# Kernel tuning notes

Measured on AMD Instinct MI355X. Metric: run time of the kernel, lower is better.

## Reference

```python
import jax, jax.numpy as jnp
import numpy as np

N, E, F_IN, H, C, L = 50000, 800000, 128, 128, 47, 3
BN_EPS = 1e-5


def setup_inputs() -> dict:
    key = jax.random.key(0)
    ks = jax.random.split(key, 12)
    s = 0.1
    return {
        "x": jax.random.normal(ks[0], (N, F_IN), jnp.float32),
        "edge_index": jax.random.randint(ks[1], (2, E), 0, N, jnp.int32),
        # stacked GINConv MLP params (in_channels == hidden so all layers stack)
        "W1": jax.random.normal(ks[2], (L, F_IN, H), jnp.float32) * s,
        "b1": jnp.full((L, H), 0.01, jnp.float32),
        "gamma": jnp.ones((L, H), jnp.float32),
        "beta": jnp.zeros((L, H), jnp.float32),
        "bn_mean": jnp.zeros((L, H), jnp.float32),
        "bn_var": jnp.ones((L, H), jnp.float32),
        "W2": jax.random.normal(ks[3], (L, H, H), jnp.float32) * s,
        "b2": jnp.full((L, H), 0.01, jnp.float32),
        # head
        "lw1": jax.random.normal(ks[4], (H, H), jnp.float32) * s,
        "lb1": jnp.zeros((H,), jnp.float32),
        "lw2": jax.random.normal(ks[5], (H, C), jnp.float32) * s,
        "lb2": jnp.zeros((C,), jnp.float32),
    }


def reference(x, edge_index, W1, b1, gamma, beta, bn_mean, bn_var, W2, b2, lw1, lb1, lw2, lb2):
    src, dst = edge_index[0], edge_index[1]
    h = x
    for i in range(L):
        # GINConv: nn((1 + eps) * x + sum_{j in N(i)} x_j), eps = 0
        agg = jax.ops.segment_sum(h[src], dst, num_segments=N)  # [N, H] scatter-sum
        z = agg + h
        z = z @ W1[i] + b1[i]
        # BatchNorm1d in eval mode (running stats)
        z = (z - bn_mean[i]) * jax.lax.rsqrt(bn_var[i] + BN_EPS) * gamma[i] + beta[i]
        z = jax.nn.relu(z)
        h = jax.nn.relu(z @ W2[i] + b2[i])
    h = jax.nn.relu(h @ lw1 + lb1)
    # dropout disabled (eval mode)
    logits = h @ lw2 + lb2
    return jax.nn.log_softmax(logits, axis=-1)
```

## Files before the change

### kernel.cpp

```cpp
#include <hip/hip_runtime.h>
#include <math.h>

#define NN 50000
#define EE 800000
#define HH 128
#define LL 3
#define CC 47
#define CAP 64
#define FILL_B 2048
#define NT_TILES 782

typedef _Float16 half8 __attribute__((ext_vector_type(8)));
typedef float    f32x4 __attribute__((ext_vector_type(4)));

__device__ __forceinline__ f32x4 mfma16(half8 a, half8 b, f32x4 c) {
    return __builtin_amdgcn_mfma_f32_16x16x32_f16(a, b, c, 0, 0, 0);
}

__global__ void k_fill_prep(const int* __restrict__ ei, int* __restrict__ cursor,
                            unsigned short* __restrict__ csr,
                            const float* __restrict__ x, const float* __restrict__ W1,
                            const float* __restrict__ W2, const float* __restrict__ lw1,
                            const float* __restrict__ lw2, const float* __restrict__ b1,
                            const float* __restrict__ gamma, const float* __restrict__ beta,
                            const float* __restrict__ bnm, const float* __restrict__ bnv,
                            _Float16* __restrict__ xh, _Float16* __restrict__ Wt1h,
                            _Float16* __restrict__ Wt2h, _Float16* __restrict__ lw1t,
                            _Float16* __restrict__ lw2t, float* __restrict__ A1f,
                            float* __restrict__ B1f) {
    if (blockIdx.x < FILL_B) {
        const int part = blockIdx.x & 7;
        const int chunk = blockIdx.x >> 3;
        const int nchunks = FILL_B >> 3;
        const int lo = part * (NN / 8);
        const int hi = (part == 7) ? NN : lo + (NN / 8);
        for (int e = chunk * 256 + threadIdx.x; e < EE; e += nchunks * 256) {
            const int d = ei[EE + e];
            if (d >= lo && d < hi) {
                const int pos = atomicAdd(&cursor[d], 1);
                if (pos < CAP) csr[(d << 6) + pos] = (unsigned short)ei[e];
            }
        }
        return;
    }
    long i = (long)(blockIdx.x - FILL_B) * 256 + threadIdx.x;
    const long P0 = (long)NN * HH;
    const long P1 = P0 + (long)LL * HH * HH;
    const long P2 = P1 + (long)LL * HH * HH;
    const long P3 = P2 + HH * HH;
    const long P4 = P3 + 48 * HH;
    const long P5 = P4 + LL * HH;
    if (i < P0) {
        xh[i] = (_Float16)x[i];
    } else if (i < P1) {
        long j = i - P0;
        int l = (int)(j / (HH * HH));
        int n = (int)((j / HH) % HH);
        int k = (int)(j % HH);
        Wt1h[l * HH * HH + n * HH + k] = (_Float16)W1[l * HH * HH + k * HH + n];
    } else if (i < P2) {
        long j = i - P1;
        int l = (int)(j / (HH * HH));
        int n = (int)((j / HH) % HH);
        int k = (int)(j % HH);
        Wt2h[l * HH * HH + n * HH + k] = (_Float16)W2[l * HH * HH + k * HH + n];
    } else if (i < P3) {
        long j = i - P2;
        int n = (int)(j / HH), k = (int)(j % HH);
        lw1t[n * HH + k] = (_Float16)lw1[k * HH + n];
    } else if (i < P4) {
        long j = i - P3;
        int n = (int)(j / HH), k = (int)(j % HH);
        lw2t[n * HH + k] = (_Float16)((n < CC) ? lw2[k * CC + n] : 0.f);
    } else if (i < P5) {
        long j = i - P4;
        float s = gamma[j] * rsqrtf(bnv[j] + 1e-5f);
        A1f[j] = s;
        B1f[j] = (b1[j] - bnm[j]) * s + beta[j];
    }
}

__global__ __launch_bounds__(256, 4) void k_layer(
    const _Float16* __restrict__ hin, _Float16* __restrict__ hout,
    const _Float16* __restrict__ Wt1, const _Float16* __restrict__ Wt2,
    const float* __restrict__ A1, const float* __restrict__ B1,
    const float* __restrict__ b2, const int* __restrict__ degs,
    const unsigned short* __restrict__ csr) {
    __shared__ _Float16 Ab[64 * 136];
    const int tid = threadIdx.x;
    const int wave = tid >> 6, lane = tid & 63;
    const int q = lane >> 4, l15 = lane & 15;
    const int tile0 = blockIdx.x * 64;
    const int fo = (tid & 15) * 8;

    half8 Bf[2][4];
#pragma unroll
    for (int t = 0; t < 2; ++t)
#pragma unroll
        for (int kt = 0; kt < 4; ++kt)
            Bf[t][kt] = *(const half8*)(Wt1 + (wave * 32 + t * 16 + l15) * 128 + kt * 32 + q * 8);

#pragma unroll
    for (int pass = 0; pass < 4; ++pass) {
        const int r = pass * 16 + (tid >> 4);
        const int g = tile0 + r;
        float a[8];
        if (g < NN) {
            half8 hv = *(const half8*)(hin + (size_t)g * HH + fo);
#pragma unroll
            for (int j = 0; j < 8; ++j) a[j] = (float)hv[j];
            int d = degs[g];
            d = (d < CAP) ? d : CAP;
            const int e0 = g << 6;
#pragma unroll 4
            for (int e = e0; e < e0 + d; ++e) {
                const int s = (int)csr[e];
                half8 v = *(const half8*)(hin + (size_t)s * HH + fo);
#pragma unroll
                for (int j = 0; j < 8; ++j) a[j] += (float)v[j];
            }
        } else {
#pragma unroll
            for (int j = 0; j < 8; ++j) a[j] = 0.f;
        }
        half8 o;
#pragma unroll
        for (int j = 0; j < 8; ++j) o[j] = (_Float16)a[j];
        *(half8*)(Ab + r * 136 + fo) = o;
    }
    __syncthreads();

    f32x4 acc[4][2];
#pragma unroll
    for (int s = 0; s < 4; ++s)
#pragma unroll
        for (int t = 0; t < 2; ++t) acc[s][t] = (f32x4){0.f, 0.f, 0.f, 0.f};
#pragma unroll
    for (int kt = 0; kt < 4; ++kt) {
        const int ko = kt * 32 + q * 8;
        half8 a0 = *(const half8*)(Ab + (0 * 16 + l15) * 136 + ko);
        half8 a1 = *(const half8*)(Ab + (1 * 16 + l15) * 136 + ko);
        half8 a2 = *(const half8*)(Ab + (2 * 16 + l15) * 136 + ko);
        half8 a3 = *(const half8*)(Ab + (3 * 16 + l15) * 136 + ko);
        acc[0][0] = mfma16(a0, Bf[0][kt], acc[0][0]);
        acc[1][0] = mfma16(a1, Bf[0][kt], acc[1][0]);
        acc[2][0] = mfma16(a2, Bf[0][kt], acc[2][0]);
        acc[3][0] = mfma16(a3, Bf[0][kt], acc[3][0]);
        acc[0][1] = mfma16(a0, Bf[1][kt], acc[0][1]);
        acc[1][1] = mfma16(a1, Bf[1][kt], acc[1][1]);
        acc[2][1] = mfma16(a2, Bf[1][kt], acc[2][1]);
        acc[3][1] = mfma16(a3, Bf[1][kt], acc[3][1]);
    }
#pragma unroll
    for (int t = 0; t < 2; ++t)
#pragma unroll
        for (int kt = 0; kt < 4; ++kt)
            Bf[t][kt] = *(const half8*)(Wt2 + (wave * 32 + t * 16 + l15) * 128 + kt * 32 + q * 8);
    __syncthreads();

#pragma unroll
    for (int t = 0; t < 2; ++t) {
        const int col = wave * 32 + t * 16 + l15;
        const float sc = A1[col], sh = B1[col];
#pragma unroll
        for (int s = 0; s < 4; ++s)
#pragma unroll
            for (int r = 0; r < 4; ++r) {
                const int row = s * 16 + q * 4 + r;
                float v = acc[s][t][r] * sc + sh;
                Ab[row * 136 + col] = (_Float16)fmaxf(v, 0.f);
            }
    }
    __syncthreads();

#pragma unroll
    for (int s = 0; s < 4; ++s)
#pragma unroll
        for (int t = 0; t < 2; ++t) acc[s][t] = (f32x4){0.f, 0.f, 0.f, 0.f};
#pragma unroll
    for (int kt = 0; kt < 4; ++kt) {
        const int ko = kt * 32 + q * 8;
        half8 a0 = *(const half8*)(Ab + (0 * 16 + l15) * 136 + ko);
        half8 a1 = *(const half8*)(Ab + (1 * 16 + l15) * 136 + ko);
        half8 a2 = *(const half8*)(Ab + (2 * 16 + l15) * 136 + ko);
        half8 a3 = *(const half8*)(Ab + (3 * 16 + l15) * 136 + ko);
        acc[0][0] = mfma16(a0, Bf[0][kt], acc[0][0]);
        acc[1][0] = mfma16(a1, Bf[0][kt], acc[1][0]);
        acc[2][0] = mfma16(a2, Bf[0][kt], acc[2][0]);
        acc[3][0] = mfma16(a3, Bf[0][kt], acc[3][0]);
        acc[0][1] = mfma16(a0, Bf[1][kt], acc[0][1]);
        acc[1][1] = mfma16(a1, Bf[1][kt], acc[1][1]);
        acc[2][1] = mfma16(a2, Bf[1][kt], acc[2][1]);
        acc[3][1] = mfma16(a3, Bf[1][kt], acc[3][1]);
    }
#pragma unroll
    for (int t = 0; t < 2; ++t) {
        const int col = wave * 32 + t * 16 + l15;
        const float bb = b2[col];
#pragma unroll
        for (int s = 0; s < 4; ++s)
#pragma unroll
            for (int r = 0; r < 4; ++r) {
                const int row = s * 16 + q * 4 + r;
                const int g = tile0 + row;
                if (g < NN) {
                    float v = fmaxf(acc[s][t][r] + bb, 0.f);
                    hout[(size_t)g * HH + col] = (_Float16)v;
                }
            }
    }
}

__global__ __launch_bounds__(256, 4) void k_layer_head(
    const _Float16* __restrict__ hin,
    const _Float16* __restrict__ Wt1, const _Float16* __restrict__ Wt2,
    const float* __restrict__ A1, const float* __restrict__ B1,
    const float* __restrict__ b2,
    const _Float16* __restrict__ lw1t, const _Float16* __restrict__ lw2t,
    const float* __restrict__ lb1, const float* __restrict__ lb2,
    float* __restrict__ out, const int* __restrict__ degs,
    const unsigned short* __restrict__ csr) {
    __shared__ _Float16 Ab[64 * 136];
    const int tid = threadIdx.x;
    const int wave = tid >> 6, lane = tid & 63;
    const int q = lane >> 4, l15 = lane & 15;
    const int tile0 = blockIdx.x * 64;
    const int fo = (tid & 15) * 8;

    half8 Bf[2][4];
#pragma unroll
    for (int t = 0; t < 2; ++t)
#pragma unroll
        for (int kt = 0; kt < 4; ++kt)
            Bf[t][kt] = *(const half8*)(Wt1 + (wave * 32 + t * 16 + l15) * 128 + kt * 32 + q * 8);

#pragma unroll
    for (int pass = 0; pass < 4; ++pass) {
        const int r = pass * 16 + (tid >> 4);
        const int g = tile0 + r;
        float a[8];
        if (g < NN) {
            half8 hv = *(const half8*)(hin + (size_t)g * HH + fo);
#pragma unroll
            for (int j = 0; j < 8; ++j) a[j] = (float)hv[j];
            int d = degs[g];
            d = (d < CAP) ? d : CAP;
            const int e0 = g << 6;
#pragma unroll 4
            for (int e = e0; e < e0 + d; ++e) {
                const int s = (int)csr[e];
                half8 v = *(const half8*)(hin + (size_t)s * HH + fo);
#pragma unroll
                for (int j = 0; j < 8; ++j) a[j] += (float)v[j];
            }
        } else {
#pragma unroll
            for (int j = 0; j < 8; ++j) a[j] = 0.f;
        }
        half8 o;
#pragma unroll
        for (int j = 0; j < 8; ++j) o[j] = (_Float16)a[j];
        *(half8*)(Ab + r * 136 + fo) = o;
    }
    __syncthreads();

    f32x4 acc[4][2];
#pragma unroll
    for (int s = 0; s < 4; ++s)
#pragma unroll
        for (int t = 0; t < 2; ++t) acc[s][t] = (f32x4){0.f, 0.f, 0.f, 0.f};
#pragma unroll
    for (int kt = 0; kt < 4; ++kt) {
        const int ko = kt * 32 + q * 8;
        half8 a0 = *(const half8*)(Ab + (0 * 16 + l15) * 136 + ko);
        half8 a1 = *(const half8*)(Ab + (1 * 16 + l15) * 136 + ko);
        half8 a2 = *(const half8*)(Ab + (2 * 16 + l15) * 136 + ko);
        half8 a3 = *(const half8*)(Ab + (3 * 16 + l15) * 136 + ko);
        acc[0][0] = mfma16(a0, Bf[0][kt], acc[0][0]);
        acc[1][0] = mfma16(a1, Bf[0][kt], acc[1][0]);
        acc[2][0] = mfma16(a2, Bf[0][kt], acc[2][0]);
        acc[3][0] = mfma16(a3, Bf[0][kt], acc[3][0]);
        acc[0][1] = mfma16(a0, Bf[1][kt], acc[0][1]);
        acc[1][1] = mfma16(a1, Bf[1][kt], acc[1][1]);
        acc[2][1] = mfma16(a2, Bf[1][kt], acc[2][1]);
        acc[3][1] = mfma16(a3, Bf[1][kt], acc[3][1]);
    }
#pragma unroll
    for (int t = 0; t < 2; ++t)
#pragma unroll
        for (int kt = 0; kt < 4; ++kt)
            Bf[t][kt] = *(const half8*)(Wt2 + (wave * 32 + t * 16 + l15) * 128 + kt * 32 + q * 8);
    __syncthreads();
#pragma unroll
    for (int t = 0; t < 2; ++t) {
        const int col = wave * 32 + t * 16 + l15;
        const float sc = A1[col], sh = B1[col];
#pragma unroll
        for (int s = 0; s < 4; ++s)
#pragma unroll
            for (int r = 0; r < 4; ++r) {
                const int row = s * 16 + q * 4 + r;
                float v = acc[s][t][r] * sc + sh;
                Ab[row * 136 + col] = (_Float16)fmaxf(v, 0.f);
            }
    }
    __syncthreads();

#pragma unroll
    for (int s = 0; s < 4; ++s)
#pragma unroll
        for (int t = 0; t < 2; ++t) acc[s][t] = (f32x4){0.f, 0.f, 0.f, 0.f};
#pragma unroll
    for (int kt = 0; kt < 4; ++kt) {
        const int ko = kt * 32 + q * 8;
        half8 a0 = *(const half8*)(Ab + (0 * 16 + l15) * 136 + ko);
        half8 a1 = *(const half8*)(Ab + (1 * 16 + l15) * 136 + ko);
        half8 a2 = *(const half8*)(Ab + (2 * 16 + l15) * 136 + ko);
        half8 a3 = *(const half8*)(Ab + (3 * 16 + l15) * 136 + ko);
        acc[0][0] = mfma16(a0, Bf[0][kt], acc[0][0]);
        acc[1][0] = mfma16(a1, Bf[0][kt], acc[1][0]);
        acc[2][0] = mfma16(a2, Bf[0][kt], acc[2][0]);
        acc[3][0] = mfma16(a3, Bf[0][kt], acc[3][0]);
        acc[0][1] = mfma16(a0, Bf[1][kt], acc[0][1]);
        acc[1][1] = mfma16(a1, Bf[1][kt], acc[1][1]);
        acc[2][1] = mfma16(a2, Bf[1][kt], acc[2][1]);
        acc[3][1] = mfma16(a3, Bf[1][kt], acc[3][1]);
    }
#pragma unroll
    for (int t = 0; t < 2; ++t)
#pragma unroll
        for (int kt = 0; kt < 4; ++kt)
            Bf[t][kt] = *(const half8*)(lw1t + (wave * 32 + t * 16 + l15) * 128 + kt * 32 + q * 8);
    __syncthreads();
#pragma unroll
    for (int t = 0; t < 2; ++t) {
        const int col = wave * 32 + t * 16 + l15;
        const float bb = b2[col];
#pragma unroll
        for (int s = 0; s < 4; ++s)
#pragma unroll
            for (int r = 0; r < 4; ++r) {
                const int row = s * 16 + q * 4 + r;
                Ab[row * 136 + col] = (_Float16)fmaxf(acc[s][t][r] + bb, 0.f);
            }
    }
    __syncthreads();

#pragma unroll
    for (int s = 0; s < 4; ++s)
#pragma unroll
        for (int t = 0; t < 2; ++t) acc[s][t] = (f32x4){0.f, 0.f, 0.f, 0.f};
#pragma unroll
    for (int kt = 0; kt < 4; ++kt) {
        const int ko = kt * 32 + q * 8;
        half8 a0 = *(const half8*)(Ab + (0 * 16 + l15) * 136 + ko);
        half8 a1 = *(const half8*)(Ab + (1 * 16 + l15) * 136 + ko);
        half8 a2 = *(const half8*)(Ab + (2 * 16 + l15) * 136 + ko);
        half8 a3 = *(const half8*)(Ab + (3 * 16 + l15) * 136 + ko);
        acc[0][0] = mfma16(a0, Bf[0][kt], acc[0][0]);
        acc[1][0] = mfma16(a1, Bf[0][kt], acc[1][0]);
        acc[2][0] = mfma16(a2, Bf[0][kt], acc[2][0]);
        acc[3][0] = mfma16(a3, Bf[0][kt], acc[3][0]);
        acc[0][1] = mfma16(a0, Bf[1][kt], acc[0][1]);
        acc[1][1] = mfma16(a1, Bf[1][kt], acc[1][1]);
        acc[2][1] = mfma16(a2, Bf[1][kt], acc[2][1]);
        acc[3][1] = mfma16(a3, Bf[1][kt], acc[3][1]);
    }
    half8 Bh[4];
    if (wave < 3) {
#pragma unroll
        for (int kt = 0; kt < 4; ++kt)
            Bh[kt] = *(const half8*)(lw2t + (wave * 16 + l15) * 128 + kt * 32 + q * 8);
    }
    __syncthreads();
#pragma unroll
    for (int t = 0; t < 2; ++t) {
        const int col = wave * 32 + t * 16 + l15;
        const float bb = lb1[col];
#pragma unroll
        for (int s = 0; s < 4; ++s)
#pragma unroll
            for (int r = 0; r < 4; ++r) {
                const int row = s * 16 + q * 4 + r;
                Ab[row * 136 + col] = (_Float16)fmaxf(acc[s][t][r] + bb, 0.f);
            }
    }
    __syncthreads();

    f32x4 acc2[4];
#pragma unroll
    for (int s = 0; s < 4; ++s) acc2[s] = (f32x4){0.f, 0.f, 0.f, 0.f};
    if (wave < 3) {
#pragma unroll
        for (int kt = 0; kt < 4; ++kt) {
            const int ko = kt * 32 + q * 8;
            half8 a0 = *(const half8*)(Ab + (0 * 16 + l15) * 136 + ko);
            half8 a1 = *(const half8*)(Ab + (1 * 16 + l15) * 136 + ko);
            half8 a2 = *(const half8*)(Ab + (2 * 16 + l15) * 136 + ko);
            half8 a3 = *(const half8*)(Ab + (3 * 16 + l15) * 136 + ko);
            acc2[0] = mfma16(a0, Bh[kt], acc2[0]);
            acc2[1] = mfma16(a1, Bh[kt], acc2[1]);
            acc2[2] = mfma16(a2, Bh[kt], acc2[2]);
            acc2[3] = mfma16(a3, Bh[kt], acc2[3]);
        }
    }
    __syncthreads();

    float* Lb = (float*)Ab;
    if (wave < 3) {
        const int col = wave * 16 + l15;
        const float bb = (col < CC) ? lb2[col] : 0.f;
#pragma unroll
        for (int s = 0; s < 4; ++s)
#pragma unroll
            for (int r = 0; r < 4; ++r) {
                const int row = s * 16 + q * 4 + r;
                Lb[row * 49 + col] = acc2[s][r] + bb;
            }
    }
    __syncthreads();

    if (tid < 64) {
        const int g = tile0 + tid;
        if (g < NN) {
            float mx = -1e30f;
            for (int c = 0; c < CC; ++c) mx = fmaxf(mx, Lb[tid * 49 + c]);
            float ssum = 0.f;
            for (int c = 0; c < CC; ++c) ssum += expf(Lb[tid * 49 + c] - mx);
            const float ls = logf(ssum) + mx;
            for (int c = 0; c < CC; ++c) out[(size_t)g * CC + c] = Lb[tid * 49 + c] - ls;
        }
    }
}

extern "C" void kernel_launch(void* const* d_in, const int* in_sizes, int n_in,
                              void* d_out, int out_size, void* d_ws, size_t ws_size,
                              hipStream_t stream) {
    const float* x     = (const float*)d_in[0];
    const int*   ei    = (const int*)d_in[1];
    const float* W1    = (const float*)d_in[2];
    const float* b1    = (const float*)d_in[3];
    const float* gamma = (const float*)d_in[4];
    const float* beta  = (const float*)d_in[5];
    const float* bnm   = (const float*)d_in[6];
    const float* bnv   = (const float*)d_in[7];
    const float* W2    = (const float*)d_in[8];
    const float* b2    = (const float*)d_in[9];
    const float* lw1   = (const float*)d_in[10];
    const float* lb1   = (const float*)d_in[11];
    const float* lw2   = (const float*)d_in[12];
    const float* lb2   = (const float*)d_in[13];
    float* out = (float*)d_out;

    char* p = (char*)d_ws;
    auto carve = [&](size_t bytes) -> char* {
        char* r = p;
        p += (bytes + 255) & ~(size_t)255;
        return r;
    };
    int* cursor = (int*)carve((size_t)NN * 4);
    unsigned short* csr = (unsigned short*)carve((size_t)NN * CAP * 2);
    _Float16* Wt1h = (_Float16*)carve((size_t)LL * HH * HH * 2);
    _Float16* Wt2h = (_Float16*)carve((size_t)LL * HH * HH * 2);
    _Float16* lw1t = (_Float16*)carve((size_t)HH * HH * 2);
    _Float16* lw2t = (_Float16*)carve((size_t)48 * HH * 2);
    float* A1f = (float*)carve((size_t)LL * HH * 4);
    float* B1f = (float*)carve((size_t)LL * HH * 4);
    _Float16* xh  = (_Float16*)carve((size_t)NN * HH * 2);
    _Float16* hb0 = (_Float16*)carve((size_t)NN * HH * 2);
    _Float16* hb1 = (_Float16*)carve((size_t)NN * HH * 2);

    hipMemsetAsync(cursor, 0, (size_t)NN * 4, stream);
    const long prep_total = (long)NN * HH + 2L * LL * HH * HH + (long)HH * HH + 48L * HH + (long)LL * HH;
    const int prep_blocks = (int)((prep_total + 255) / 256);
    k_fill_prep<<<FILL_B + prep_blocks, 256, 0, stream>>>(
        ei, cursor, csr, x, W1, W2, lw1, lw2, b1, gamma, beta, bnm, bnv,
        xh, Wt1h, Wt2h, lw1t, lw2t, A1f, B1f);

    k_layer<<<NT_TILES, 256, 0, stream>>>(xh, hb0, Wt1h, Wt2h, A1f, B1f, b2,
                                          cursor, csr);
    k_layer<<<NT_TILES, 256, 0, stream>>>(hb0, hb1, Wt1h + HH * HH, Wt2h + HH * HH,
                                          A1f + HH, B1f + HH, b2 + HH,
                                          cursor, csr);
    k_layer_head<<<NT_TILES, 256, 0, stream>>>(hb1, Wt1h + 2 * HH * HH, Wt2h + 2 * HH * HH,
                                               A1f + 2 * HH, B1f + 2 * HH, b2 + 2 * HH,
                                               lw1t, lw2t, lb1, lb2, out,
                                               cursor, csr);
}
```

Before: 275.3 us.

## Halve node tile, batch neighbor gathers by four with zero sentinel row

Shrinks each block's node tile from 64 to 32 rows, doubling the number of blocks and raising the launch-bounds occupancy hint, so more blocks run concurrently to hide gather latency. The neighbor aggregation now reads four CSR indices at once and issues four independent row loads per step. Out-of-range slots point at an extra zero row appended to each feature buffer, which the prep kernel clears. The x-to-half conversion is also vectorized to eight elements per thread. The trade-off is that each block reloads the weight fragments for half as many rows, and padded slots cost wasted loads.

```diff
diff --git a/kernel.cpp b/kernel.cpp
--- a/kernel.cpp
+++ b/kernel.cpp
@@ -8,10 +8,12 @@
 #define CC 47
 #define CAP 64
 #define FILL_B 2048
-#define NT_TILES 782
+#define TILE 32
+#define NT_TILES 1563
 
 typedef _Float16 half8 __attribute__((ext_vector_type(8)));
 typedef float    f32x4 __attribute__((ext_vector_type(4)));
+typedef unsigned short us4 __attribute__((ext_vector_type(4)));
 
 __device__ __forceinline__ f32x4 mfma16(half8 a, half8 b, f32x4 c) {
     return __builtin_amdgcn_mfma_f32_16x16x32_f16(a, b, c, 0, 0, 0);
@@ -24,7 +26,8 @@
                             const float* __restrict__ lw2, const float* __restrict__ b1,
                             const float* __restrict__ gamma, const float* __restrict__ beta,
                             const float* __restrict__ bnm, const float* __restrict__ bnv,
-                            _Float16* __restrict__ xh, _Float16* __restrict__ Wt1h,
+                            _Float16* __restrict__ xh, _Float16* __restrict__ hb0,
+                            _Float16* __restrict__ hb1, _Float16* __restrict__ Wt1h,
                             _Float16* __restrict__ Wt2h, _Float16* __restrict__ lw1t,
                             _Float16* __restrict__ lw2t, float* __restrict__ A1f,
                             float* __restrict__ B1f) {
@@ -43,54 +46,65 @@
         }
         return;
     }
-    long i = (long)(blockIdx.x - FILL_B) * 256 + threadIdx.x;
-    const long P0 = (long)NN * HH;
-    const long P1 = P0 + (long)LL * HH * HH;
-    const long P2 = P1 + (long)LL * HH * HH;
-    const long P3 = P2 + HH * HH;
-    const long P4 = P3 + 48 * HH;
-    const long P5 = P4 + LL * HH;
-    if (i < P0) {
-        xh[i] = (_Float16)x[i];
-    } else if (i < P1) {
-        long j = i - P0;
-        int l = (int)(j / (HH * HH));
-        int n = (int)((j / HH) % HH);
-        int k = (int)(j % HH);
+    const int i = (blockIdx.x - FILL_B) * 256 + threadIdx.x;
+    const int Q0 = (NN * HH) / 8;
+    const int Q1 = Q0 + LL * HH * HH;
+    const int Q2 = Q1 + LL * HH * HH;
+    const int Q3 = Q2 + HH * HH;
+    const int Q4 = Q3 + 48 * HH;
+    const int Q5 = Q4 + LL * HH;
+    const int Q6 = Q5 + 3 * HH;
+    if (i < Q0) {
+        const f32x4* xp = (const f32x4*)x + (size_t)i * 2;
+        f32x4 u = xp[0], v = xp[1];
+        half8 o;
+        o[0] = (_Float16)u[0]; o[1] = (_Float16)u[1]; o[2] = (_Float16)u[2]; o[3] = (_Float16)u[3];
+        o[4] = (_Float16)v[0]; o[5] = (_Float16)v[1]; o[6] = (_Float16)v[2]; o[7] = (_Float16)v[3];
+        *((half8*)xh + i) = o;
+    } else if (i < Q1) {
+        int j = i - Q0;
+        int l = j / (HH * HH);
+        int n = (j / HH) % HH;
+        int k = j % HH;
         Wt1h[l * HH * HH + n * HH + k] = (_Float16)W1[l * HH * HH + k * HH + n];
-    } else if (i < P2) {
-        long j = i - P1;
-        int l = (int)(j / (HH * HH));
-        int n = (int)((j / HH) % HH);
-        int k = (int)(j % HH);
+    } else if (i < Q2) {
+        int j = i - Q1;
+        int l = j / (HH * HH);
+        int n = (j / HH) % HH;
+        int k = j % HH;
         Wt2h[l * HH * HH + n * HH + k] = (_Float16)W2[l * HH * HH + k * HH + n];
-    } else if (i < P3) {
-        long j = i - P2;
-        int n = (int)(j / HH), k = (int)(j % HH);
+    } else if (i < Q3) {
+        int j = i - Q2;
+        int n = j / HH, k = j % HH;
         lw1t[n * HH + k] = (_Float16)lw1[k * HH + n];
-    } else if (i < P4) {
-        long j = i - P3;
-        int n = (int)(j / HH), k = (int)(j % HH);
+    } else if (i < Q4) {
+        int j = i - Q3;
+        int n = j / HH, k = j % HH;
         lw2t[n * HH + k] = (_Float16)((n < CC) ? lw2[k * CC + n] : 0.f);
-    } else if (i < P5) {
-        long j = i - P4;
+    } else if (i < Q5) {
+        int j = i - Q4;
         float s = gamma[j] * rsqrtf(bnv[j] + 1e-5f);
         A1f[j] = s;
         B1f[j] = (b1[j] - bnm[j]) * s + beta[j];
+    } else if (i < Q6) {
+        int j = i - Q5;
+        int b = j >> 7, k = j & 127;
+        _Float16* t = (b == 0) ? xh : ((b == 1) ? hb0 : hb1);
+        t[(size_t)NN * HH + k] = (_Float16)0.f;
     }
 }
 
-__global__ __launch_bounds__(256, 4) void k_layer(
+__global__ __launch_bounds__(256, 6) void k_layer(
     const _Float16* __restrict__ hin, _Float16* __restrict__ hout,
     const _Float16* __restrict__ Wt1, const _Float16* __restrict__ Wt2,
     const float* __restrict__ A1, const float* __restrict__ B1,
     const float* __restrict__ b2, const int* __restrict__ degs,
     const unsigned short* __restrict__ csr) {
-    __shared__ _Float16 Ab[64 * 136];
+    __shared__ _Float16 Ab[TILE * 136];
     const int tid = threadIdx.x;
     const int wave = tid >> 6, lane = tid & 63;
     const int q = lane >> 4, l15 = lane & 15;
-    const int tile0 = blockIdx.x * 64;
+    const int tile0 = blockIdx.x * TILE;
     const int fo = (tid & 15) * 8;
 
     half8 Bf[2][4];
@@ -101,27 +115,30 @@
             Bf[t][kt] = *(const half8*)(Wt1 + (wave * 32 + t * 16 + l15) * 128 + kt * 32 + q * 8);
 
 #pragma unroll
-    for (int pass = 0; pass < 4; ++pass) {
+    for (int pass = 0; pass < 2; ++pass) {
         const int r = pass * 16 + (tid >> 4);
         const int g = tile0 + r;
+        const int gg = (g < NN) ? g : NN;
         float a[8];
-        if (g < NN) {
-            half8 hv = *(const half8*)(hin + (size_t)g * HH + fo);
-#pragma unroll
-            for (int j = 0; j < 8; ++j) a[j] = (float)hv[j];
-            int d = degs[g];
-            d = (d < CAP) ? d : CAP;
-            const int e0 = g << 6;
-#pragma unroll 4
-            for (int e = e0; e < e0 + d; ++e) {
-                const int s = (int)csr[e];
-                half8 v = *(const half8*)(hin + (size_t)s * HH + fo);
-#pragma unroll
-                for (int j = 0; j < 8; ++j) a[j] += (float)v[j];
-            }
-        } else {
-#pragma unroll
-            for (int j = 0; j < 8; ++j) a[j] = 0.f;
+        half8 hv = *(const half8*)(hin + (size_t)gg * HH + fo);
+#pragma unroll
+        for (int j = 0; j < 8; ++j) a[j] = (float)hv[j];
+        int d = (g < NN) ? degs[g] : 0;
+        d = (d < CAP) ? d : CAP;
+        const int e0 = gg << 6;
+        for (int c = 0; c < d; c += 4) {
+            us4 sv = *(const us4*)(csr + e0 + c);
+            const int s0 = (int)sv[0];
+            const int s1 = (c + 1 < d) ? (int)sv[1] : NN;
+            const int s2 = (c + 2 < d) ? (int)sv[2] : NN;
+            const int s3 = (c + 3 < d) ? (int)sv[3] : NN;
+            half8 v0 = *(const half8*)(hin + (size_t)s0 * HH + fo);
+            half8 v1 = *(const half8*)(hin + (size_t)s1 * HH + fo);
+            half8 v2 = *(const half8*)(hin + (size_t)s2 * HH + fo);
+            half8 v3 = *(const half8*)(hin + (size_t)s3 * HH + fo);
+#pragma unroll
+            for (int j = 0; j < 8; ++j)
+                a[j] += ((float)v0[j] + (float)v1[j]) + ((float)v2[j] + (float)v3[j]);
         }
         half8 o;
 #pragma unroll
@@ -130,9 +147,9 @@
     }
     __syncthreads();
 
-    f32x4 acc[4][2];
-#pragma unroll
-    for (int s = 0; s < 4; ++s)
+    f32x4 acc[2][2];
+#pragma unroll
+    for (int s = 0; s < 2; ++s)
 #pragma unroll
         for (int t = 0; t < 2; ++t) acc[s][t] = (f32x4){0.f, 0.f, 0.f, 0.f};
 #pragma unroll
@@ -140,16 +157,10 @@
         const int ko = kt * 32 + q * 8;
         half8 a0 = *(const half8*)(Ab + (0 * 16 + l15) * 136 + ko);
         half8 a1 = *(const half8*)(Ab + (1 * 16 + l15) * 136 + ko);
-        half8 a2 = *(const half8*)(Ab + (2 * 16 + l15) * 136 + ko);
-        half8 a3 = *(const half8*)(Ab + (3 * 16 + l15) * 136 + ko);
         acc[0][0] = mfma16(a0, Bf[0][kt], acc[0][0]);
         acc[1][0] = mfma16(a1, Bf[0][kt], acc[1][0]);
-        acc[2][0] = mfma16(a2, Bf[0][kt], acc[2][0]);
-        acc[3][0] = mfma16(a3, Bf[0][kt], acc[3][0]);
         acc[0][1] = mfma16(a0, Bf[1][kt], acc[0][1]);
         acc[1][1] = mfma16(a1, Bf[1][kt], acc[1][1]);
-        acc[2][1] = mfma16(a2, Bf[1][kt], acc[2][1]);
-        acc[3][1] = mfma16(a3, Bf[1][kt], acc[3][1]);
     }
 #pragma unroll
     for (int t = 0; t < 2; ++t)
@@ -163,7 +174,7 @@
         const int col = wave * 32 + t * 16 + l15;
         const float sc = A1[col], sh = B1[col];
 #pragma unroll
-        for (int s = 0; s < 4; ++s)
+        for (int s = 0; s < 2; ++s)
 #pragma unroll
             for (int r = 0; r < 4; ++r) {
                 const int row = s * 16 + q * 4 + r;
@@ -174,7 +185,7 @@
     __syncthreads();
 
 #pragma unroll
-    for (int s = 0; s < 4; ++s)
+    for (int s = 0; s < 2; ++s)
 #pragma unroll
         for (int t = 0; t < 2; ++t) acc[s][t] = (f32x4){0.f, 0.f, 0.f, 0.f};
 #pragma unroll
@@ -182,23 +193,17 @@
         const int ko = kt * 32 + q * 8;
         half8 a0 = *(const half8*)(Ab + (0 * 16 + l15) * 136 + ko);
         half8 a1 = *(const half8*)(Ab + (1 * 16 + l15) * 136 + ko);
-        half8 a2 = *(const half8*)(Ab + (2 * 16 + l15) * 136 + ko);
-        half8 a3 = *(const half8*)(Ab + (3 * 16 + l15) * 136 + ko);
         acc[0][0] = mfma16(a0, Bf[0][kt], acc[0][0]);
         acc[1][0] = mfma16(a1, Bf[0][kt], acc[1][0]);
-        acc[2][0] = mfma16(a2, Bf[0][kt], acc[2][0]);
-        acc[3][0] = mfma16(a3, Bf[0][kt], acc[3][0]);
         acc[0][1] = mfma16(a0, Bf[1][kt], acc[0][1]);
         acc[1][1] = mfma16(a1, Bf[1][kt], acc[1][1]);
-        acc[2][1] = mfma16(a2, Bf[1][kt], acc[2][1]);
-        acc[3][1] = mfma16(a3, Bf[1][kt], acc[3][1]);
     }
 #pragma unroll
     for (int t = 0; t < 2; ++t) {
         const int col = wave * 32 + t * 16 + l15;
         const float bb = b2[col];
 #pragma unroll
-        for (int s = 0; s < 4; ++s)
+        for (int s = 0; s < 2; ++s)
 #pragma unroll
             for (int r = 0; r < 4; ++r) {
                 const int row = s * 16 + q * 4 + r;
@@ -211,7 +216,7 @@
     }
 }
 
-__global__ __launch_bounds__(256, 4) void k_layer_head(
+__global__ __launch_bounds__(256, 6) void k_layer_head(
     const _Float16* __restrict__ hin,
     const _Float16* __restrict__ Wt1, const _Float16* __restrict__ Wt2,
     const float* __restrict__ A1, const float* __restrict__ B1,
@@ -220,11 +225,11 @@
     const float* __restrict__ lb1, const float* __restrict__ lb2,
     float* __restrict__ out, const int* __restrict__ degs,
     const unsigned short* __restrict__ csr) {
-    __shared__ _Float16 Ab[64 * 136];
+    __shared__ _Float16 Ab[TILE * 136];
     const int tid = threadIdx.x;
     const int wave = tid >> 6, lane = tid & 63;
     const int q = lane >> 4, l15 = lane & 15;
-    const int tile0 = blockIdx.x * 64;
+    const int tile0 = blockIdx.x * TILE;
     const int fo = (tid & 15) * 8;
 
     half8 Bf[2][4];
@@ -235,27 +240,30 @@
             Bf[t][kt] = *(const half8*)(Wt1 + (wave * 32 + t * 16 + l15) * 128 + kt * 32 + q * 8);
 
 #pragma unroll
-    for (int pass = 0; pass < 4; ++pass) {
+    for (int pass = 0; pass < 2; ++pass) {
         const int r = pass * 16 + (tid >> 4);
         const int g = tile0 + r;
+        const int gg = (g < NN) ? g : NN;
         float a[8];
-        if (g < NN) {
-            half8 hv = *(const half8*)(hin + (size_t)g * HH + fo);
-#pragma unroll
-            for (int j = 0; j < 8; ++j) a[j] = (float)hv[j];
-            int d = degs[g];
-            d = (d < CAP) ? d : CAP;
-            const int e0 = g << 6;
-#pragma unroll 4
-            for (int e = e0; e < e0 + d; ++e) {
-                const int s = (int)csr[e];
-                half8 v = *(const half8*)(hin + (size_t)s * HH + fo);
-#pragma unroll
-                for (int j = 0; j < 8; ++j) a[j] += (float)v[j];
-            }
-        } else {
-#pragma unroll
-            for (int j = 0; j < 8; ++j) a[j] = 0.f;
+        half8 hv = *(const half8*)(hin + (size_t)gg * HH + fo);
+#pragma unroll
+        for (int j = 0; j < 8; ++j) a[j] = (float)hv[j];
+        int d = (g < NN) ? degs[g] : 0;
+        d = (d < CAP) ? d : CAP;
+        const int e0 = gg << 6;
+        for (int c = 0; c < d; c += 4) {
+            us4 sv = *(const us4*)(csr + e0 + c);
+            const int s0 = (int)sv[0];
+            const int s1 = (c + 1 < d) ? (int)sv[1] : NN;
+            const int s2 = (c + 2 < d) ? (int)sv[2] : NN;
+            const int s3 = (c + 3 < d) ? (int)sv[3] : NN;
+            half8 v0 = *(const half8*)(hin + (size_t)s0 * HH + fo);
+            half8 v1 = *(const half8*)(hin + (size_t)s1 * HH + fo);
+            half8 v2 = *(const half8*)(hin + (size_t)s2 * HH + fo);
+            half8 v3 = *(const half8*)(hin + (size_t)s3 * HH + fo);
+#pragma unroll
+            for (int j = 0; j < 8; ++j)
+                a[j] += ((float)v0[j] + (float)v1[j]) + ((float)v2[j] + (float)v3[j]);
         }
         half8 o;
 #pragma unroll
@@ -264,9 +272,9 @@
     }
     __syncthreads();
 
-    f32x4 acc[4][2];
-#pragma unroll
-    for (int s = 0; s < 4; ++s)
+    f32x4 acc[2][2];
+#pragma unroll
+    for (int s = 0; s < 2; ++s)
 #pragma unroll
         for (int t = 0; t < 2; ++t) acc[s][t] = (f32x4){0.f, 0.f, 0.f, 0.f};
 #pragma unroll
@@ -274,16 +282,10 @@
         const int ko = kt * 32 + q * 8;
         half8 a0 = *(const half8*)(Ab + (0 * 16 + l15) * 136 + ko);
         half8 a1 = *(const half8*)(Ab + (1 * 16 + l15) * 136 + ko);
-        half8 a2 = *(const half8*)(Ab + (2 * 16 + l15) * 136 + ko);
-        half8 a3 = *(const half8*)(Ab + (3 * 16 + l15) * 136 + ko);
         acc[0][0] = mfma16(a0, Bf[0][kt], acc[0][0]);
         acc[1][0] = mfma16(a1, Bf[0][kt], acc[1][0]);
-        acc[2][0] = mfma16(a2, Bf[0][kt], acc[2][0]);
-        acc[3][0] = mfma16(a3, Bf[0][kt], acc[3][0]);
         acc[0][1] = mfma16(a0, Bf[1][kt], acc[0][1]);
         acc[1][1] = mfma16(a1, Bf[1][kt], acc[1][1]);
-        acc[2][1] = mfma16(a2, Bf[1][kt], acc[2][1]);
-        acc[3][1] = mfma16(a3, Bf[1][kt], acc[3][1]);
     }
 #pragma unroll
     for (int t = 0; t < 2; ++t)
@@ -296,7 +298,7 @@
         const int col = wave * 32 + t * 16 + l15;
         const float sc = A1[col], sh = B1[col];
 #pragma unroll
-        for (int s = 0; s < 4; ++s)
+        for (int s = 0; s < 2; ++s)
 #pragma unroll
             for (int r = 0; r < 4; ++r) {
                 const int row = s * 16 + q * 4 + r;
@@ -307,7 +309,7 @@
     __syncthreads();
 
 #pragma unroll
-    for (int s = 0; s < 4; ++s)
+    for (int s = 0; s < 2; ++s)
 #pragma unroll
         for (int t = 0; t < 2; ++t) acc[s][t] = (f32x4){0.f, 0.f, 0.f, 0.f};
 #pragma unroll
@@ -315,16 +317,10 @@
         const int ko = kt * 32 + q * 8;
         half8 a0 = *(const half8*)(Ab + (0 * 16 + l15) * 136 + ko);
         half8 a1 = *(const half8*)(Ab + (1 * 16 + l15) * 136 + ko);
-        half8 a2 = *(const half8*)(Ab + (2 * 16 + l15) * 136 + ko);
-        half8 a3 = *(const half8*)(Ab + (3 * 16 + l15) * 136 + ko);
         acc[0][0] = mfma16(a0, Bf[0][kt], acc[0][0]);
         acc[1][0] = mfma16(a1, Bf[0][kt], acc[1][0]);
-        acc[2][0] = mfma16(a2, Bf[0][kt], acc[2][0]);
-        acc[3][0] = mfma16(a3, Bf[0][kt], acc[3][0]);
         acc[0][1] = mfma16(a0, Bf[1][kt], acc[0][1]);
         acc[1][1] = mfma16(a1, Bf[1][kt], acc[1][1]);
-        acc[2][1] = mfma16(a2, Bf[1][kt], acc[2][1]);
-        acc[3][1] = mfma16(a3, Bf[1][kt], acc[3][1]);
     }
 #pragma unroll
     for (int t = 0; t < 2; ++t)
@@ -337,7 +333,7 @@
         const int col = wave * 32 + t * 16 + l15;
         const float bb = b2[col];
 #pragma unroll
-        for (int s = 0; s < 4; ++s)
+        for (int s = 0; s < 2; ++s)
 #pragma unroll
             for (int r = 0; r < 4; ++r) {
                 const int row = s * 16 + q * 4 + r;
@@ -347,7 +343,7 @@
     __syncthreads();
 
 #pragma unroll
-    for (int s = 0; s < 4; ++s)
+    for (int s = 0; s < 2; ++s)
 #pragma unroll
         for (int t = 0; t < 2; ++t) acc[s][t] = (f32x4){0.f, 0.f, 0.f, 0.f};
 #pragma unroll
@@ -355,16 +351,10 @@
         const int ko = kt * 32 + q * 8;
         half8 a0 = *(const half8*)(Ab + (0 * 16 + l15) * 136 + ko);
         half8 a1 = *(const half8*)(Ab + (1 * 16 + l15) * 136 + ko);
-        half8 a2 = *(const half8*)(Ab + (2 * 16 + l15) * 136 + ko);
-        half8 a3 = *(const half8*)(Ab + (3 * 16 + l15) * 136 + ko);
         acc[0][0] = mfma16(a0, Bf[0][kt], acc[0][0]);
         acc[1][0] = mfma16(a1, Bf[0][kt], acc[1][0]);
-        acc[2][0] = mfma16(a2, Bf[0][kt], acc[2][0]);
-        acc[3][0] = mfma16(a3, Bf[0][kt], acc[3][0]);
         acc[0][1] = mfma16(a0, Bf[1][kt], acc[0][1]);
         acc[1][1] = mfma16(a1, Bf[1][kt], acc[1][1]);
-        acc[2][1] = mfma16(a2, Bf[1][kt], acc[2][1]);
-        acc[3][1] = mfma16(a3, Bf[1][kt], acc[3][1]);
     }
     half8 Bh[4];
     if (wave < 3) {
@@ -378,7 +368,7 @@
         const int col = wave * 32 + t * 16 + l15;
         const float bb = lb1[col];
 #pragma unroll
-        for (int s = 0; s < 4; ++s)
+        for (int s = 0; s < 2; ++s)
 #pragma unroll
             for (int r = 0; r < 4; ++r) {
                 const int row = s * 16 + q * 4 + r;
@@ -387,21 +377,17 @@
     }
     __syncthreads();
 
-    f32x4 acc2[4];
-#pragma unroll
-    for (int s = 0; s < 4; ++s) acc2[s] = (f32x4){0.f, 0.f, 0.f, 0.f};
+    f32x4 acc2[2];
+#pragma unroll
+    for (int s = 0; s < 2; ++s) acc2[s] = (f32x4){0.f, 0.f, 0.f, 0.f};
     if (wave < 3) {
 #pragma unroll
         for (int kt = 0; kt < 4; ++kt) {
             const int ko = kt * 32 + q * 8;
             half8 a0 = *(const half8*)(Ab + (0 * 16 + l15) * 136 + ko);
             half8 a1 = *(const half8*)(Ab + (1 * 16 + l15) * 136 + ko);
-            half8 a2 = *(const half8*)(Ab + (2 * 16 + l15) * 136 + ko);
-            half8 a3 = *(const half8*)(Ab + (3 * 16 + l15) * 136 + ko);
             acc2[0] = mfma16(a0, Bh[kt], acc2[0]);
             acc2[1] = mfma16(a1, Bh[kt], acc2[1]);
-            acc2[2] = mfma16(a2, Bh[kt], acc2[2]);
-            acc2[3] = mfma16(a3, Bh[kt], acc2[3]);
         }
     }
     __syncthreads();
@@ -411,7 +397,7 @@
         const int col = wave * 16 + l15;
         const float bb = (col < CC) ? lb2[col] : 0.f;
 #pragma unroll
-        for (int s = 0; s < 4; ++s)
+        for (int s = 0; s < 2; ++s)
 #pragma unroll
             for (int r = 0; r < 4; ++r) {
                 const int row = s * 16 + q * 4 + r;
@@ -420,7 +406,7 @@
     }
     __syncthreads();
 
-    if (tid < 64) {
+    if (tid < TILE) {
         const int g = tile0 + tid;
         if (g < NN) {
             float mx = -1e30f;
@@ -466,16 +452,16 @@
     _Float16* lw2t = (_Float16*)carve((size_t)48 * HH * 2);
     float* A1f = (float*)carve((size_t)LL * HH * 4);
     float* B1f = (float*)carve((size_t)LL * HH * 4);
-    _Float16* xh  = (_Float16*)carve((size_t)NN * HH * 2);
-    _Float16* hb0 = (_Float16*)carve((size_t)NN * HH * 2);
-    _Float16* hb1 = (_Float16*)carve((size_t)NN * HH * 2);
+    _Float16* xh  = (_Float16*)carve((size_t)(NN + 1) * HH * 2);
+    _Float16* hb0 = (_Float16*)carve((size_t)(NN + 1) * HH * 2);
+    _Float16* hb1 = (_Float16*)carve((size_t)(NN + 1) * HH * 2);
 
     hipMemsetAsync(cursor, 0, (size_t)NN * 4, stream);
-    const long prep_total = (long)NN * HH + 2L * LL * HH * HH + (long)HH * HH + 48L * HH + (long)LL * HH;
-    const int prep_blocks = (int)((prep_total + 255) / 256);
+    const int prep_total = (NN * HH) / 8 + 2 * LL * HH * HH + HH * HH + 48 * HH + LL * HH + 3 * HH;
+    const int prep_blocks = (prep_total + 255) / 256;
     k_fill_prep<<<FILL_B + prep_blocks, 256, 0, stream>>>(
         ei, cursor, csr, x, W1, W2, lw1, lw2, b1, gamma, beta, bnm, bnv,
-        xh, Wt1h, Wt2h, lw1t, lw2t, A1f, B1f);
+        xh, hb0, hb1, Wt1h, Wt2h, lw1t, lw2t, A1f, B1f);
 
     k_layer<<<NT_TILES, 256, 0, stream>>>(xh, hb0, Wt1h, Wt2h, A1f, B1f, b2,
                                           cursor, csr);
```

Result: slower. 294.1 us (+6.8%).

## Batch neighbor gathers eight at a time with zero sentinel row; vectorize x conversion

Applied to the files above, without the earlier changes.

The neighbor aggregation now loads eight CSR indices at once as a vector and issues eight independent row loads before accumulating. Out-of-range slots point at an extra zero row appended to each feature buffer, so the inner loop needs no branches. The goal is more memory-level parallelism in the latency-bound gather. The prep kernel also converts x to fp16 eight elements per thread and writes the sentinel zero rows. In exchange, padded slots issue wasted loads for nodes whose degree is not a multiple of eight, and register pressure rises.

```diff
diff --git a/kernel.cpp b/kernel.cpp
--- a/kernel.cpp
+++ b/kernel.cpp
@@ -12,6 +12,7 @@
 
 typedef _Float16 half8 __attribute__((ext_vector_type(8)));
 typedef float    f32x4 __attribute__((ext_vector_type(4)));
+typedef unsigned short us8 __attribute__((ext_vector_type(8)));
 
 __device__ __forceinline__ f32x4 mfma16(half8 a, half8 b, f32x4 c) {
     return __builtin_amdgcn_mfma_f32_16x16x32_f16(a, b, c, 0, 0, 0);
@@ -24,7 +25,8 @@
                             const float* __restrict__ lw2, const float* __restrict__ b1,
                             const float* __restrict__ gamma, const float* __restrict__ beta,
                             const float* __restrict__ bnm, const float* __restrict__ bnv,
-                            _Float16* __restrict__ xh, _Float16* __restrict__ Wt1h,
+                            _Float16* __restrict__ xh, _Float16* __restrict__ hb0,
+                            _Float16* __restrict__ hb1, _Float16* __restrict__ Wt1h,
                             _Float16* __restrict__ Wt2h, _Float16* __restrict__ lw1t,
                             _Float16* __restrict__ lw2t, float* __restrict__ A1f,
                             float* __restrict__ B1f) {
@@ -43,40 +45,87 @@
         }
         return;
     }
-    long i = (long)(blockIdx.x - FILL_B) * 256 + threadIdx.x;
-    const long P0 = (long)NN * HH;
-    const long P1 = P0 + (long)LL * HH * HH;
-    const long P2 = P1 + (long)LL * HH * HH;
-    const long P3 = P2 + HH * HH;
-    const long P4 = P3 + 48 * HH;
-    const long P5 = P4 + LL * HH;
-    if (i < P0) {
-        xh[i] = (_Float16)x[i];
-    } else if (i < P1) {
-        long j = i - P0;
-        int l = (int)(j / (HH * HH));
-        int n = (int)((j / HH) % HH);
-        int k = (int)(j % HH);
+    const int i = (blockIdx.x - FILL_B) * 256 + threadIdx.x;
+    const int Q0 = (NN * HH) / 8;
+    const int Q1 = Q0 + LL * HH * HH;
+    const int Q2 = Q1 + LL * HH * HH;
+    const int Q3 = Q2 + HH * HH;
+    const int Q4 = Q3 + 48 * HH;
+    const int Q5 = Q4 + LL * HH;
+    const int Q6 = Q5 + 3 * HH;
+    if (i < Q0) {
+        const f32x4* xp = (const f32x4*)x + (size_t)i * 2;
+        f32x4 u = xp[0], v = xp[1];
+        half8 o;
+        o[0] = (_Float16)u[0]; o[1] = (_Float16)u[1]; o[2] = (_Float16)u[2]; o[3] = (_Float16)u[3];
+        o[4] = (_Float16)v[0]; o[5] = (_Float16)v[1]; o[6] = (_Float16)v[2]; o[7] = (_Float16)v[3];
+        *((half8*)xh + i) = o;
+    } else if (i < Q1) {
+        int j = i - Q0;
+        int l = j / (HH * HH);
+        int n = (j / HH) % HH;
+        int k = j % HH;
         Wt1h[l * HH * HH + n * HH + k] = (_Float16)W1[l * HH * HH + k * HH + n];
-    } else if (i < P2) {
-        long j = i - P1;
-        int l = (int)(j / (HH * HH));
-        int n = (int)((j / HH) % HH);
-        int k = (int)(j % HH);
+    } else if (i < Q2) {
+        int j = i - Q1;
+        int l = j / (HH * HH);
+        int n = (j / HH) % HH;
+        int k = j % HH;
         Wt2h[l * HH * HH + n * HH + k] = (_Float16)W2[l * HH * HH + k * HH + n];
-    } else if (i < P3) {
-        long j = i - P2;
-        int n = (int)(j / HH), k = (int)(j % HH);
+    } else if (i < Q3) {
+        int j = i - Q2;
+        int n = j / HH, k = j % HH;
         lw1t[n * HH + k] = (_Float16)lw1[k * HH + n];
-    } else if (i < P4) {
-        long j = i - P3;
-        int n = (int)(j / HH), k = (int)(j % HH);
+    } else if (i < Q4) {
+        int j = i - Q3;
+        int n = j / HH, k = j % HH;
         lw2t[n * HH + k] = (_Float16)((n < CC) ? lw2[k * CC + n] : 0.f);
-    } else if (i < P5) {
-        long j = i - P4;
+    } else if (i < Q5) {
+        int j = i - Q4;
         float s = gamma[j] * rsqrtf(bnv[j] + 1e-5f);
         A1f[j] = s;
         B1f[j] = (b1[j] - bnm[j]) * s + beta[j];
+    } else if (i < Q6) {
+        int j = i - Q5;
+        int b = j >> 7, k = j & 127;
+        _Float16* t = (b == 0) ? xh : ((b == 1) ? hb0 : hb1);
+        t[(size_t)NN * HH + k] = (_Float16)0.f;
+    }
+}
+
+__device__ __forceinline__ void gather_tile(
+    const _Float16* __restrict__ hin, const int* __restrict__ degs,
+    const unsigned short* __restrict__ csr, _Float16* Ab, int tile0, int tid, int fo) {
+#pragma unroll
+    for (int pass = 0; pass < 4; ++pass) {
+        const int r = pass * 16 + (tid >> 4);
+        const int g = tile0 + r;
+        const int gg = (g < NN) ? g : NN;
+        float a[8];
+        half8 hv = *(const half8*)(hin + (size_t)gg * HH + fo);
+#pragma unroll
+        for (int j = 0; j < 8; ++j) a[j] = (float)hv[j];
+        int d = (g < NN) ? degs[g] : 0;
+        d = (d < CAP) ? d : CAP;
+        const unsigned short* crow = csr + (gg << 6);
+        for (int kk = 0; kk < d; kk += 8) {
+            us8 sv = *(const us8*)(crow + kk);
+            int s[8];
+#pragma unroll
+            for (int j = 0; j < 8; ++j) s[j] = (kk + j < d) ? (int)sv[j] : NN;
+            half8 v[8];
+#pragma unroll
+            for (int j = 0; j < 8; ++j) v[j] = *(const half8*)(hin + (size_t)s[j] * HH + fo);
+#pragma unroll
+            for (int j = 0; j < 8; ++j) {
+#pragma unroll
+                for (int t = 0; t < 8; ++t) a[t] += (float)v[j][t];
+            }
+        }
+        half8 o;
+#pragma unroll
+        for (int j = 0; j < 8; ++j) o[j] = (_Float16)a[j];
+        *(half8*)(Ab + r * 136 + fo) = o;
     }
 }
 
@@ -100,34 +149,7 @@
         for (int kt = 0; kt < 4; ++kt)
             Bf[t][kt] = *(const half8*)(Wt1 + (wave * 32 + t * 16 + l15) * 128 + kt * 32 + q * 8);
 
-#pragma unroll
-    for (int pass = 0; pass < 4; ++pass) {
-        const int r = pass * 16 + (tid >> 4);
-        const int g = tile0 + r;
-        float a[8];
-        if (g < NN) {
-            half8 hv = *(const half8*)(hin + (size_t)g * HH + fo);
-#pragma unroll
-            for (int j = 0; j < 8; ++j) a[j] = (float)hv[j];
-            int d = degs[g];
-            d = (d < CAP) ? d : CAP;
-            const int e0 = g << 6;
-#pragma unroll 4
-            for (int e = e0; e < e0 + d; ++e) {
-                const int s = (int)csr[e];
-                half8 v = *(const half8*)(hin + (size_t)s * HH + fo);
-#pragma unroll
-                for (int j = 0; j < 8; ++j) a[j] += (float)v[j];
-            }
-        } else {
-#pragma unroll
-            for (int j = 0; j < 8; ++j) a[j] = 0.f;
-        }
-        half8 o;
-#pragma unroll
-        for (int j = 0; j < 8; ++j) o[j] = (_Float16)a[j];
-        *(half8*)(Ab + r * 136 + fo) = o;
-    }
+    gather_tile(hin, degs, csr, Ab, tile0, tid, fo);
     __syncthreads();
 
     f32x4 acc[4][2];
@@ -234,34 +256,7 @@
         for (int kt = 0; kt < 4; ++kt)
             Bf[t][kt] = *(const half8*)(Wt1 + (wave * 32 + t * 16 + l15) * 128 + kt * 32 + q * 8);
 
-#pragma unroll
-    for (int pass = 0; pass < 4; ++pass) {
-        const int r = pass * 16 + (tid >> 4);
-        const int g = tile0 + r;
-        float a[8];
-        if (g < NN) {
-            half8 hv = *(const half8*)(hin + (size_t)g * HH + fo);
-#pragma unroll
-            for (int j = 0; j < 8; ++j) a[j] = (float)hv[j];
-            int d = degs[g];
-            d = (d < CAP) ? d : CAP;
-            const int e0 = g << 6;
-#pragma unroll 4
-            for (int e = e0; e < e0 + d; ++e) {
-                const int s = (int)csr[e];
-                half8 v = *(const half8*)(hin + (size_t)s * HH + fo);
-#pragma unroll
-                for (int j = 0; j < 8; ++j) a[j] += (float)v[j];
-            }
-        } else {
-#pragma unroll
-            for (int j = 0; j < 8; ++j) a[j] = 0.f;
-        }
-        half8 o;
-#pragma unroll
-        for (int j = 0; j < 8; ++j) o[j] = (_Float16)a[j];
-        *(half8*)(Ab + r * 136 + fo) = o;
-    }
+    gather_tile(hin, degs, csr, Ab, tile0, tid, fo);
     __syncthreads();
 
     f32x4 acc[4][2];
@@ -466,16 +461,16 @@
     _Float16* lw2t = (_Float16*)carve((size_t)48 * HH * 2);
     float* A1f = (float*)carve((size_t)LL * HH * 4);
     float* B1f = (float*)carve((size_t)LL * HH * 4);
-    _Float16* xh  = (_Float16*)carve((size_t)NN * HH * 2);
-    _Float16* hb0 = (_Float16*)carve((size_t)NN * HH * 2);
-    _Float16* hb1 = (_Float16*)carve((size_t)NN * HH * 2);
+    _Float16* xh  = (_Float16*)carve((size_t)(NN + 1) * HH * 2);
+    _Float16* hb0 = (_Float16*)carve((size_t)(NN + 1) * HH * 2);
+    _Float16* hb1 = (_Float16*)carve((size_t)(NN + 1) * HH * 2);
 
     hipMemsetAsync(cursor, 0, (size_t)NN * 4, stream);
-    const long prep_total = (long)NN * HH + 2L * LL * HH * HH + (long)HH * HH + 48L * HH + (long)LL * HH;
-    const int prep_blocks = (int)((prep_total + 255) / 256);
+    const int prep_total = (NN * HH) / 8 + 2 * LL * HH * HH + HH * HH + 48 * HH + LL * HH + 3 * HH;
+    const int prep_blocks = (prep_total + 255) / 256;
     k_fill_prep<<<FILL_B + prep_blocks, 256, 0, stream>>>(
         ei, cursor, csr, x, W1, W2, lw1, lw2, b1, gamma, beta, bnm, bnv,
-        xh, Wt1h, Wt2h, lw1t, lw2t, A1f, B1f);
+        xh, hb0, hb1, Wt1h, Wt2h, lw1t, lw2t, A1f, B1f);
 
     k_layer<<<NT_TILES, 256, 0, stream>>>(xh, hb0, Wt1h, Wt2h, A1f, B1f, b2,
                                           cursor, csr);
```

Result: faster. 266.6 us (-3.2%).
